# Kernel optimization log

Measured on AMD Instinct MI355X. Metric: run time of the kernel, lower is better.

## Reference

```python
import jax, jax.numpy as jnp
import numpy as np

B, N, L, D, V = 1024, 50, 50, 128, 500000
STEPS = 1  # args['n_layers']


def setup_inputs() -> dict:
    key = jax.random.key(0)
    ks = jax.random.split(key, 26)
    s = 1.0 / np.sqrt(D)  # SRGNN._init_weights uniform(-stdv, stdv)
    u = lambda k, shape: jax.random.uniform(k, shape, jnp.float32, -s, s)
    return {
        'items': jax.random.randint(ks[0], (B, N), 0, V),
        'A': jax.random.uniform(ks[1], (B, N, 2 * N), jnp.float32),
        'alias_inputs': jax.random.randint(ks[2], (B, L), 0, N),
        'mask': jnp.ones((B, L), dtype=bool),
        'lens': jax.random.randint(ks[3], (B,), 1, L + 1),
        'emb': u(ks[4], (V, D)),
        'w_ih': u(ks[5], (3 * D, 2 * D)),
        'w_hh': u(ks[6], (3 * D, D)),
        'b_ih': u(ks[7], (3 * D,)),
        'b_hh': u(ks[8], (3 * D,)),
        'b_iah': u(ks[9], (D,)),
        'b_oah': u(ks[10], (D,)),
        'w_in': u(ks[11], (D, D)),
        'bi_in': u(ks[12], (D,)),
        'w_out': u(ks[13], (D, D)),
        'bi_out': u(ks[14], (D,)),
        'w1': u(ks[15], (D, D)),
        'b1': u(ks[16], (D,)),
        'w2': u(ks[17], (D, D)),
        'b2': u(ks[18], (D,)),
        'w3': u(ks[19], (D, D)),
        'b3': u(ks[20], (D,)),
        'wt': u(ks[21], (D, 2 * D)),
        'bt': u(ks[22], (D,)),
    }


def reference(items, A, alias_inputs, mask, lens, emb, w_ih, w_hh, b_ih, b_hh,
              b_iah, b_oah, w_in, bi_in, w_out, bi_out, w1, b1, w2, b2, w3, b3,
              wt, bt):
    hidden = emb[items]  # [B, N, D]
    a_in, a_out = A[:, :, :N], A[:, :, N:]
    for _ in range(STEPS):
        # gated GNN cell (GRU-style)
        inp_in = jnp.einsum('bij,bjd->bid', a_in, hidden @ w_in.T + bi_in) + b_iah
        inp_out = jnp.einsum('bij,bjd->bid', a_out, hidden @ w_out.T + bi_out) + b_oah
        gi = jnp.concatenate([inp_in, inp_out], axis=-1) @ w_ih.T + b_ih  # [B,N,3D]
        gh = hidden @ w_hh.T + b_hh  # [B,N,3D]
        i_r, i_i, i_n = jnp.split(gi, 3, axis=-1)
        h_r, h_i, h_n = jnp.split(gh, 3, axis=-1)
        resetgate = jax.nn.sigmoid(i_r + h_r)
        inputgate = jax.nn.sigmoid(i_i + h_i)
        newgate = jnp.tanh(i_n + resetgate * h_n)
        hidden = newgate + inputgate * (hidden - newgate)
    # gather per-position node hidden states
    seq_hidden = jnp.take_along_axis(hidden, alias_inputs[:, :, None], axis=1)  # [B,L,D]
    # last valid item
    ht = jnp.take_along_axis(seq_hidden, (lens - 1)[:, None, None], axis=1)[:, 0, :]  # [B,D]
    # sigmoid attention combine
    q1 = (ht @ w1.T + b1)[:, None, :]            # [B,1,D]
    q2 = seq_hidden @ w2.T + b2                  # [B,L,D]
    alp = jax.nn.sigmoid(q1 + q2) @ w3.T + b3    # [B,L,D]
    a = jnp.sum(alp * seq_hidden * mask[:, :, None].astype(jnp.float32), axis=1)
    seq_output = jnp.concatenate([a, ht], axis=-1) @ wt.T + bt  # [B,D]
    return (seq_hidden, seq_output)
```

## Files before the change

### kernel.cpp

```cpp
#include <hip/hip_runtime.h>
#include <math.h>

#define TB 512

typedef __attribute__((ext_vector_type(8))) short bf16x8;
typedef __attribute__((ext_vector_type(4))) float f32x4;

__device__ __forceinline__ float u2f(unsigned short u){
  union { unsigned int i; float f; } v; v.i = ((unsigned int)u) << 16; return v.f;
}
__device__ __forceinline__ unsigned short f2u(float f){
  union { float ff; unsigned int i; } v; v.ff = f;
  unsigned int x = v.i;
  x += 0x7fff + ((x >> 16) & 1);
  return (unsigned short)(x >> 16);
}
__device__ __forceinline__ float sigm(float x){
  return __builtin_amdgcn_rcpf(1.0f + __expf(-x));
}
__device__ __forceinline__ float ftanh(float x){
  return 1.0f - 2.0f*__builtin_amdgcn_rcpf(1.0f + __expf(2.0f*x));
}

#define SH 136
#define ST 72
#define OFF_H    0
#define OFF_II   6800
#define OFF_IO   13600
#define OFF_HT   20400
#define OFF_AIN  29616
#define OFF_AOUT 33216
#define POOL_SZ  37824

#define WOFF_IN   0
#define WOFF_OUT  16384
#define WOFF_IH   32768
#define WOFF_HH   131072
#define WOFF_W2   180224
#define WOFF_W3   196608
#define WTOT      212992

__device__ __forceinline__ f32x4 mfma16(bf16x8 a, bf16x8 b, f32x4 c){
  return __builtin_amdgcn_mfma_f32_16x16x32_bf16(a, b, c, 0, 0, 0);
}

__device__ __forceinline__ bf16x8 cvt8(const float* __restrict__ p){
  const float4 a = *(const float4*)p;
  const float4 c = *(const float4*)(p + 4);
  bf16x8 r;
  r[0]=(short)f2u(a.x); r[1]=(short)f2u(a.y); r[2]=(short)f2u(a.z); r[3]=(short)f2u(a.w);
  r[4]=(short)f2u(c.x); r[5]=(short)f2u(c.y); r[6]=(short)f2u(c.z); r[7]=(short)f2u(c.w);
  return r;
}

__device__ __forceinline__ void gemm_frag(const unsigned short* sA, int lda,
                                          const unsigned short* sB, int ldb,
                                          int n0, int lane, int nk, f32x4 acc[4]){
  const int l15 = lane & 15, q = lane >> 4;
  for (int ks = 0; ks < nk; ++ks){
    const int k0 = ks*32 + q*8;
    bf16x8 bfr = *(const bf16x8*)(sB + (n0 + l15)*ldb + k0);
    #pragma unroll
    for (int mt = 0; mt < 4; ++mt){
      bf16x8 afr = *(const bf16x8*)(sA + (mt*16 + l15)*lda + k0);
      acc[mt] = mfma16(afr, bfr, acc[mt]);
    }
  }
}

__device__ __forceinline__ void gemm_fragB(const unsigned short* sA, int lda,
                                           const unsigned short* __restrict__ Wb, int ldw,
                                           int n0, int lane, int nk, f32x4 acc[4]){
  const int l15 = lane & 15, q = lane >> 4;
  const unsigned short* wr = Wb + (n0 + l15)*ldw;
  for (int ks = 0; ks < nk; ++ks){
    const int k0 = ks*32 + q*8;
    bf16x8 bfr = *(const bf16x8*)(wr + k0);
    #pragma unroll
    for (int mt = 0; mt < 4; ++mt){
      bf16x8 afr = *(const bf16x8*)(sA + (mt*16 + l15)*lda + k0);
      acc[mt] = mfma16(afr, bfr, acc[mt]);
    }
  }
}

__device__ __forceinline__ void gemm_fragG(const unsigned short* sA, int lda,
                                           const float* __restrict__ W, int ldw,
                                           int n0, int lane, int nk, f32x4 acc[4]){
  const int l15 = lane & 15, q = lane >> 4;
  const float* wr = W + (n0 + l15)*ldw;
  for (int ks = 0; ks < nk; ++ks){
    const int k0 = ks*32 + q*8;
    bf16x8 bfr = cvt8(wr + k0);
    #pragma unroll
    for (int mt = 0; mt < 4; ++mt){
      bf16x8 afr = *(const bf16x8*)(sA + (mt*16 + l15)*lda + k0);
      acc[mt] = mfma16(afr, bfr, acc[mt]);
    }
  }
}

__global__ void prep_weights(const float* __restrict__ w_in, const float* __restrict__ w_out,
                             const float* __restrict__ w_ih, const float* __restrict__ w_hh,
                             const float* __restrict__ w2,   const float* __restrict__ w3,
                             unsigned short* __restrict__ ws){
  const int i = blockIdx.x*blockDim.x + threadIdx.x;
  const int s = gridDim.x*blockDim.x;
  for (int e = i; e < 16384; e += s) ws[WOFF_IN  + e] = f2u(w_in[e]);
  for (int e = i; e < 16384; e += s) ws[WOFF_OUT + e] = f2u(w_out[e]);
  for (int e = i; e < 98304; e += s) ws[WOFF_IH  + e] = f2u(w_ih[e]);
  for (int e = i; e < 49152; e += s) ws[WOFF_HH  + e] = f2u(w_hh[e]);
  for (int e = i; e < 16384; e += s) ws[WOFF_W2  + e] = f2u(w2[e]);
  for (int e = i; e < 16384; e += s) ws[WOFF_W3  + e] = f2u(w3[e]);
}

template<bool WS>
__global__ __launch_bounds__(TB, 4) void srgnn_kernel(
    const int* __restrict__ items, const float* __restrict__ A,
    const int* __restrict__ alias_in, const int* __restrict__ lens,
    const float* __restrict__ emb,
    const float* __restrict__ w_ih, const float* __restrict__ w_hh,
    const float* __restrict__ b_ih, const float* __restrict__ b_hh,
    const float* __restrict__ b_iah, const float* __restrict__ b_oah,
    const float* __restrict__ w_in, const float* __restrict__ bi_in,
    const float* __restrict__ w_out, const float* __restrict__ bi_out,
    const float* __restrict__ w1, const float* __restrict__ b1,
    const float* __restrict__ w2, const float* __restrict__ b2,
    const float* __restrict__ w3, const float* __restrict__ b3,
    const float* __restrict__ wt, const float* __restrict__ bt,
    const unsigned short* __restrict__ wbf,
    float* __restrict__ out0, float* __restrict__ out1)
{
  __shared__ __align__(16) unsigned short pool[POOL_SZ];

  const int b    = blockIdx.x;
  const int tid  = threadIdx.x;
  const int lane = tid & 63;
  const int w    = tid >> 6;
  const int n0   = w << 4;
  const int l15  = lane & 15, q = lane >> 4;
  const int d    = n0 + l15;

  unsigned short* pH   = pool + OFF_H;
  unsigned short* pII  = pool + OFF_II;
  unsigned short* pIO  = pool + OFF_IO;
  unsigned short* pHT  = pool + OFF_HT;
  unsigned short* pAin = pool + OFF_AIN;
  unsigned short* pAout= pool + OFF_AOUT;
  unsigned short* pHn  = pool + OFF_AIN;
  float* sQ1  = (float*)(pool + OFF_HT);
  float* sAvec = sQ1 + 128;
  float* sAred = sQ1 + 256;

  for (int e = tid; e < 1792; e += TB){
    int r_ = e/14; pHT[r_*ST + 50 + (e - r_*14)] = 0;
  }
  for (int e = tid; e < 700; e += TB){
    int r_ = e/14, c = 50 + (e - r_*14);
    pAin[r_*ST + c] = 0; pAout[r_*ST + c] = 0;
  }

  for (int e = tid; e < 1250; e += TB){
    int i = e/25, j4 = (e - i*25) << 2;
    const float4 v = *(const float4*)(A + (long long)b*5000 + i*100 + j4);
    const float vv[4] = {v.x, v.y, v.z, v.w};
    #pragma unroll
    for (int t = 0; t < 4; ++t){
      int j = j4 + t;
      if (j < 50) pAin[i*ST + j] = f2u(vv[t]);
      else        pAout[i*ST + j - 50] = f2u(vv[t]);
    }
  }
  for (int e = tid; e < 1600; e += TB){
    int n = e >> 5, c4 = (e & 31) << 2;
    const float4 v = *(const float4*)(emb + (long long)items[b*50 + n]*128 + c4);
    unsigned short* p = pH + n*SH + c4;
    p[0] = f2u(v.x); p[1] = f2u(v.y); p[2] = f2u(v.z); p[3] = f2u(v.w);
  }
  __syncthreads();

  f32x4 acc[4];

  { const float bi = bi_in[d];
    #pragma unroll
    for (int mt = 0; mt < 4; ++mt) acc[mt] = (f32x4){bi,bi,bi,bi};
    if (WS) gemm_fragB(pH, SH, wbf + WOFF_IN, 128, n0, lane, 4, acc);
    else    gemm_fragG(pH, SH, w_in, 128, n0, lane, 4, acc);
    #pragma unroll
    for (int mt = 0; mt < 4; ++mt)
      #pragma unroll
      for (int r = 0; r < 4; ++r){
        int tok = mt*16 + q*4 + r;
        if (tok < 50) pHT[d*ST + tok] = f2u(acc[mt][r]);
      }
  }
  { const float bi = b_iah[d];
    #pragma unroll
    for (int mt = 0; mt < 4; ++mt) acc[mt] = (f32x4){bi,bi,bi,bi};
    gemm_frag(pAin, ST, pHT, ST, n0, lane, 2, acc);
    #pragma unroll
    for (int mt = 0; mt < 4; ++mt)
      #pragma unroll
      for (int r = 0; r < 4; ++r){
        int tok = mt*16 + q*4 + r;
        if (tok < 50) pII[tok*SH + d] = f2u(acc[mt][r]);
      }
  }
  { const float bi = bi_out[d];
    #pragma unroll
    for (int mt = 0; mt < 4; ++mt) acc[mt] = (f32x4){bi,bi,bi,bi};
    if (WS) gemm_fragB(pH, SH, wbf + WOFF_OUT, 128, n0, lane, 4, acc);
    else    gemm_fragG(pH, SH, w_out, 128, n0, lane, 4, acc);
    #pragma unroll
    for (int mt = 0; mt < 4; ++mt)
      #pragma unroll
      for (int r = 0; r < 4; ++r){
        int tok = mt*16 + q*4 + r;
        if (tok < 50) pHT[d*ST + tok] = f2u(acc[mt][r]);
      }
  }
  { const float bi = b_oah[d];
    #pragma unroll
    for (int mt = 0; mt < 4; ++mt) acc[mt] = (f32x4){bi,bi,bi,bi};
    gemm_frag(pAout, ST, pHT, ST, n0, lane, 2, acc);
    #pragma unroll
    for (int mt = 0; mt < 4; ++mt)
      #pragma unroll
      for (int r = 0; r < 4; ++r){
        int tok = mt*16 + q*4 + r;
        if (tok < 50) pIO[tok*SH + d] = f2u(acc[mt][r]);
      }
  }
  __syncthreads();

  unsigned int Rp[8], Zp[8];
  for (int g = 0; g < 3; ++g){
    f32x4 agi[4], agh[4];
    { const float bii = b_ih[g*128 + d], bhh = b_hh[g*128 + d];
      #pragma unroll
      for (int mt = 0; mt < 4; ++mt){
        agi[mt] = (f32x4){bii,bii,bii,bii};
        agh[mt] = (f32x4){bhh,bhh,bhh,bhh};
      }
    }
    if (WS){
      gemm_fragB(pII, SH, wbf + WOFF_IH + g*128*256,       256, n0, lane, 4, agi);
      gemm_fragB(pIO, SH, wbf + WOFF_IH + g*128*256 + 128, 256, n0, lane, 4, agi);
      gemm_fragB(pH,  SH, wbf + WOFF_HH + g*128*128,       128, n0, lane, 4, agh);
    } else {
      gemm_fragG(pII, SH, w_ih + g*128*256,       256, n0, lane, 4, agi);
      gemm_fragG(pIO, SH, w_ih + g*128*256 + 128, 256, n0, lane, 4, agi);
      gemm_fragG(pH,  SH, w_hh + g*128*128,       128, n0, lane, 4, agh);
    }

    #pragma unroll
    for (int mt = 0; mt < 4; ++mt)
      #pragma unroll
      for (int r2 = 0; r2 < 2; ++r2){
        const int p = mt*2 + r2;
        if (g == 0){
          float v0 = sigm(agi[mt][2*r2]   + agh[mt][2*r2]);
          float v1 = sigm(agi[mt][2*r2+1] + agh[mt][2*r2+1]);
          Rp[p] = (unsigned)f2u(v0) | ((unsigned)f2u(v1) << 16);
        } else if (g == 1){
          float v0 = sigm(agi[mt][2*r2]   + agh[mt][2*r2]);
          float v1 = sigm(agi[mt][2*r2+1] + agh[mt][2*r2+1]);
          Zp[p] = (unsigned)f2u(v0) | ((unsigned)f2u(v1) << 16);
        } else {
          #pragma unroll
          for (int rr = 0; rr < 2; ++rr){
            const int r = 2*r2 + rr;
            const int tok = mt*16 + q*4 + r;
            if (tok < 50){
              float Rv = u2f((unsigned short)(Rp[p] >> (rr*16)));
              float Zv = u2f((unsigned short)(Zp[p] >> (rr*16)));
              float h  = u2f(pH[tok*SH + d]);
              float ng = ftanh(agi[mt][r] + Rv*agh[mt][r]);
              pHn[tok*128 + d] = f2u(ng + Zv*(h - ng));
            }
          }
        }
      }
  }
  __syncthreads();

  for (int e = tid; e < 1600; e += TB){
    int l = e >> 5, c4 = (e & 31) << 2;
    const uint2 v = *(const uint2*)(pHn + alias_in[b*50 + l]*128 + c4);
    *(uint2*)(pH + l*SH + c4) = v;
    float4 o;
    o.x = u2f((unsigned short)(v.x)); o.y = u2f((unsigned short)(v.x >> 16));
    o.z = u2f((unsigned short)(v.y)); o.w = u2f((unsigned short)(v.y >> 16));
    *(float4*)(out0 + (long long)b*6400 + 4*e) = o;
  }
  const int hl = lens[b] - 1;
  __syncthreads();

  if (tid < 128){
    float q1v = b1[tid];
    for (int k = 0; k < 128; k += 4){
      const float4 wv = *(const float4*)(w1 + tid*128 + k);
      q1v += wv.x*u2f(pH[hl*SH + k])   + wv.y*u2f(pH[hl*SH + k+1])
           + wv.z*u2f(pH[hl*SH + k+2]) + wv.w*u2f(pH[hl*SH + k+3]);
    }
    sQ1[tid] = q1v;
  }
  { const float bi = b2[d];
    #pragma unroll
    for (int mt = 0; mt < 4; ++mt) acc[mt] = (f32x4){bi,bi,bi,bi};
    if (WS) gemm_fragB(pH, SH, wbf + WOFF_W2, 128, n0, lane, 4, acc);
    else    gemm_fragG(pH, SH, w2, 128, n0, lane, 4, acc);
    __syncthreads();
    const float q1v = sQ1[d];
    #pragma unroll
    for (int mt = 0; mt < 4; ++mt)
      #pragma unroll
      for (int r = 0; r < 4; ++r){
        int tok = mt*16 + q*4 + r;
        if (tok < 50) pII[tok*SH + d] = f2u(sigm(q1v + acc[mt][r]));
      }
  }
  __syncthreads();

  { const float bi = b3[d];
    #pragma unroll
    for (int mt = 0; mt < 4; ++mt) acc[mt] = (f32x4){bi,bi,bi,bi};
    if (WS) gemm_fragB(pII, SH, wbf + WOFF_W3, 128, n0, lane, 4, acc);
    else    gemm_fragG(pII, SH, w3, 128, n0, lane, 4, acc);
    float pa = 0.f;
    #pragma unroll
    for (int mt = 0; mt < 4; ++mt)
      #pragma unroll
      for (int r = 0; r < 4; ++r){
        int tok = mt*16 + q*4 + r;
        if (tok < 50) pa += acc[mt][r] * u2f(pH[tok*SH + d]);
      }
    pa += __shfl_xor(pa, 16);
    pa += __shfl_xor(pa, 32);
    if (lane < 16) sAvec[n0 + lane] = pa;
  }
  __syncthreads();

  { const int dd = tid & 127, gg = tid >> 7;
    float part = (gg == 0) ? bt[dd] : 0.f;
    if (gg < 2){
      for (int kk = 0; kk < 64; kk += 4){
        int k = gg*64 + kk;
        const float4 wv = *(const float4*)(wt + dd*256 + k);
        part += wv.x*sAvec[k] + wv.y*sAvec[k+1] + wv.z*sAvec[k+2] + wv.w*sAvec[k+3];
      }
    } else {
      for (int kk = 0; kk < 64; kk += 4){
        int k = (gg - 2)*64 + kk;
        const float4 wv = *(const float4*)(wt + dd*256 + 128 + k);
        part += wv.x*u2f(pH[hl*SH + k])   + wv.y*u2f(pH[hl*SH + k+1])
              + wv.z*u2f(pH[hl*SH + k+2]) + wv.w*u2f(pH[hl*SH + k+3]);
      }
    }
    sAred[gg*128 + dd] = part;
  }
  __syncthreads();
  if (tid < 128)
    out1[(long long)b*128 + tid] = sAred[tid] + sAred[128+tid] + sAred[256+tid] + sAred[384+tid];
}

extern "C" void kernel_launch(void* const* d_in, const int* in_sizes, int n_in,
                              void* d_out, int out_size, void* d_ws, size_t ws_size,
                              hipStream_t stream){
  float* out0 = (float*)d_out;
  float* out1 = out0 + 1024LL*50*128;
  const bool ws_ok = (d_ws != nullptr) && (ws_size >= (size_t)WTOT*2);
  if (ws_ok){
    prep_weights<<<256, 256, 0, stream>>>(
        (const float*)d_in[12], (const float*)d_in[14],
        (const float*)d_in[6],  (const float*)d_in[7],
        (const float*)d_in[18], (const float*)d_in[20],
        (unsigned short*)d_ws);
    srgnn_kernel<true><<<1024, TB, 0, stream>>>(
        (const int*)d_in[0], (const float*)d_in[1], (const int*)d_in[2],
        (const int*)d_in[4],
        (const float*)d_in[5],
        (const float*)d_in[6], (const float*)d_in[7], (const float*)d_in[8],
        (const float*)d_in[9], (const float*)d_in[10], (const float*)d_in[11],
        (const float*)d_in[12], (const float*)d_in[13], (const float*)d_in[14],
        (const float*)d_in[15], (const float*)d_in[16], (const float*)d_in[17],
        (const float*)d_in[18], (const float*)d_in[19], (const float*)d_in[20],
        (const float*)d_in[21], (const float*)d_in[22], (const float*)d_in[23],
        (const unsigned short*)d_ws, out0, out1);
  } else {
    srgnn_kernel<false><<<1024, TB, 0, stream>>>(
        (const int*)d_in[0], (const float*)d_in[1], (const int*)d_in[2],
        (const int*)d_in[4],
        (const float*)d_in[5],
        (const float*)d_in[6], (const float*)d_in[7], (const float*)d_in[8],
        (const float*)d_in[9], (const float*)d_in[10], (const float*)d_in[11],
        (const float*)d_in[12], (const float*)d_in[13], (const float*)d_in[14],
        (const float*)d_in[15], (const float*)d_in[16], (const float*)d_in[17],
        (const float*)d_in[18], (const float*)d_in[19], (const float*)d_in[20],
        (const float*)d_in[21], (const float*)d_in[22], (const float*)d_in[23],
        nullptr, out0, out1);
  }
}
```

Baseline: 465.8 us.

## Double block size and split token tiles across two wave groups

```diff
diff --git a/kernel.cpp b/kernel.cpp
--- a/kernel.cpp
+++ b/kernel.cpp
@@ -1,7 +1,7 @@
 #include <hip/hip_runtime.h>
 #include <math.h>
 
-#define TB 512
+#define TB 1024
 
 typedef __attribute__((ext_vector_type(8))) short bf16x8;
 typedef __attribute__((ext_vector_type(4))) float f32x4;
@@ -53,49 +53,47 @@
   return r;
 }
 
-__device__ __forceinline__ void gemm_frag(const unsigned short* sA, int lda,
-                                          const unsigned short* sB, int ldb,
-                                          int n0, int lane, int nk, f32x4 acc[4]){
+__device__ __forceinline__ void gemm2L(const unsigned short* sA, int lda, int mbase,
+                                       const unsigned short* sB, int ldb,
+                                       int n0, int lane, int nk, f32x4 acc[2]){
   const int l15 = lane & 15, q = lane >> 4;
   for (int ks = 0; ks < nk; ++ks){
     const int k0 = ks*32 + q*8;
     bf16x8 bfr = *(const bf16x8*)(sB + (n0 + l15)*ldb + k0);
     #pragma unroll
-    for (int mt = 0; mt < 4; ++mt){
-      bf16x8 afr = *(const bf16x8*)(sA + (mt*16 + l15)*lda + k0);
-      acc[mt] = mfma16(afr, bfr, acc[mt]);
-    }
-  }
-}
-
-__device__ __forceinline__ void gemm_fragB(const unsigned short* sA, int lda,
-                                           const unsigned short* __restrict__ Wb, int ldw,
-                                           int n0, int lane, int nk, f32x4 acc[4]){
+    for (int mtl = 0; mtl < 2; ++mtl){
+      bf16x8 afr = *(const bf16x8*)(sA + (mbase + mtl*16 + l15)*lda + k0);
+      acc[mtl] = mfma16(afr, bfr, acc[mtl]);
+    }
+  }
+}
+__device__ __forceinline__ void gemm2B(const unsigned short* sA, int lda, int mbase,
+                                       const unsigned short* __restrict__ Wb, int ldw,
+                                       int n0, int lane, int nk, f32x4 acc[2]){
   const int l15 = lane & 15, q = lane >> 4;
   const unsigned short* wr = Wb + (n0 + l15)*ldw;
   for (int ks = 0; ks < nk; ++ks){
     const int k0 = ks*32 + q*8;
     bf16x8 bfr = *(const bf16x8*)(wr + k0);
     #pragma unroll
-    for (int mt = 0; mt < 4; ++mt){
-      bf16x8 afr = *(const bf16x8*)(sA + (mt*16 + l15)*lda + k0);
-      acc[mt] = mfma16(afr, bfr, acc[mt]);
-    }
-  }
-}
-
-__device__ __forceinline__ void gemm_fragG(const unsigned short* sA, int lda,
-                                           const float* __restrict__ W, int ldw,
-                                           int n0, int lane, int nk, f32x4 acc[4]){
+    for (int mtl = 0; mtl < 2; ++mtl){
+      bf16x8 afr = *(const bf16x8*)(sA + (mbase + mtl*16 + l15)*lda + k0);
+      acc[mtl] = mfma16(afr, bfr, acc[mtl]);
+    }
+  }
+}
+__device__ __forceinline__ void gemm2G(const unsigned short* sA, int lda, int mbase,
+                                       const float* __restrict__ W, int ldw,
+                                       int n0, int lane, int nk, f32x4 acc[2]){
   const int l15 = lane & 15, q = lane >> 4;
   const float* wr = W + (n0 + l15)*ldw;
   for (int ks = 0; ks < nk; ++ks){
     const int k0 = ks*32 + q*8;
     bf16x8 bfr = cvt8(wr + k0);
     #pragma unroll
-    for (int mt = 0; mt < 4; ++mt){
-      bf16x8 afr = *(const bf16x8*)(sA + (mt*16 + l15)*lda + k0);
-      acc[mt] = mfma16(afr, bfr, acc[mt]);
+    for (int mtl = 0; mtl < 2; ++mtl){
+      bf16x8 afr = *(const bf16x8*)(sA + (mbase + mtl*16 + l15)*lda + k0);
+      acc[mtl] = mfma16(afr, bfr, acc[mtl]);
     }
   }
 }
@@ -115,7 +113,7 @@
 }
 
 template<bool WS>
-__global__ __launch_bounds__(TB, 4) void srgnn_kernel(
+__global__ __launch_bounds__(TB, 8) void srgnn_kernel(
     const int* __restrict__ items, const float* __restrict__ A,
     const int* __restrict__ alias_in, const int* __restrict__ lens,
     const float* __restrict__ emb,
@@ -137,7 +135,9 @@
   const int tid  = threadIdx.x;
   const int lane = tid & 63;
   const int w    = tid >> 6;
-  const int n0   = w << 4;
+  const int n0   = (w & 7) << 4;
+  const int mh   = w >> 3;
+  const int mbase= mh << 5;
   const int l15  = lane & 15, q = lane >> 4;
   const int d    = n0 + l15;
 
@@ -148,9 +148,10 @@
   unsigned short* pAin = pool + OFF_AIN;
   unsigned short* pAout= pool + OFF_AOUT;
   unsigned short* pHn  = pool + OFF_AIN;
-  float* sQ1  = (float*)(pool + OFF_HT);
-  float* sAvec = sQ1 + 128;
-  float* sAred = sQ1 + 256;
+  float* sQ1   = (float*)(pool + OFF_HT);
+  float* sAvec0= sQ1 + 128;
+  float* sAvec1= sQ1 + 256;
+  float* sAred = sQ1 + 384;
 
   for (int e = tid; e < 1792; e += TB){
     int r_ = e/14; pHT[r_*ST + 50 + (e - r_*14)] = 0;
@@ -179,103 +180,130 @@
   }
   __syncthreads();
 
-  f32x4 acc[4];
-
-  { const float bi = bi_in[d];
-    #pragma unroll
-    for (int mt = 0; mt < 4; ++mt) acc[mt] = (f32x4){bi,bi,bi,bi};
-    if (WS) gemm_fragB(pH, SH, wbf + WOFF_IN, 128, n0, lane, 4, acc);
-    else    gemm_fragG(pH, SH, w_in, 128, n0, lane, 4, acc);
-    #pragma unroll
-    for (int mt = 0; mt < 4; ++mt)
-      #pragma unroll
-      for (int r = 0; r < 4; ++r){
-        int tok = mt*16 + q*4 + r;
-        if (tok < 50) pHT[d*ST + tok] = f2u(acc[mt][r]);
-      }
-  }
+  f32x4 acc[2];
+
+  f32x4 aO[2];
+  { const float biI = bi_in[d], biO = bi_out[d];
+    acc[0] = (f32x4){biI,biI,biI,biI}; acc[1] = acc[0];
+    aO[0]  = (f32x4){biO,biO,biO,biO}; aO[1]  = aO[0];
+    if (WS){
+      const unsigned short* wI = wbf + WOFF_IN  + (n0 + l15)*128;
+      const unsigned short* wO = wbf + WOFF_OUT + (n0 + l15)*128;
+      #pragma unroll
+      for (int ks = 0; ks < 4; ++ks){
+        const int k0 = ks*32 + q*8;
+        bf16x8 bI = *(const bf16x8*)(wI + k0);
+        bf16x8 bO = *(const bf16x8*)(wO + k0);
+        #pragma unroll
+        for (int mtl = 0; mtl < 2; ++mtl){
+          bf16x8 afr = *(const bf16x8*)(pH + (mbase + mtl*16 + l15)*SH + k0);
+          acc[mtl] = mfma16(afr, bI, acc[mtl]);
+          aO[mtl]  = mfma16(afr, bO, aO[mtl]);
+        }
+      }
+    } else {
+      const float* wI = w_in  + (n0 + l15)*128;
+      const float* wO = w_out + (n0 + l15)*128;
+      #pragma unroll
+      for (int ks = 0; ks < 4; ++ks){
+        const int k0 = ks*32 + q*8;
+        bf16x8 bI = cvt8(wI + k0);
+        bf16x8 bO = cvt8(wO + k0);
+        #pragma unroll
+        for (int mtl = 0; mtl < 2; ++mtl){
+          bf16x8 afr = *(const bf16x8*)(pH + (mbase + mtl*16 + l15)*SH + k0);
+          acc[mtl] = mfma16(afr, bI, acc[mtl]);
+          aO[mtl]  = mfma16(afr, bO, aO[mtl]);
+        }
+      }
+    }
+    #pragma unroll
+    for (int mtl = 0; mtl < 2; ++mtl)
+      #pragma unroll
+      for (int r = 0; r < 4; ++r){
+        int tok = mbase + mtl*16 + q*4 + r;
+        if (tok < 50) pHT[d*ST + tok] = f2u(acc[mtl][r]);
+      }
+  }
+  __syncthreads();
+
   { const float bi = b_iah[d];
-    #pragma unroll
-    for (int mt = 0; mt < 4; ++mt) acc[mt] = (f32x4){bi,bi,bi,bi};
-    gemm_frag(pAin, ST, pHT, ST, n0, lane, 2, acc);
-    #pragma unroll
-    for (int mt = 0; mt < 4; ++mt)
-      #pragma unroll
-      for (int r = 0; r < 4; ++r){
-        int tok = mt*16 + q*4 + r;
-        if (tok < 50) pII[tok*SH + d] = f2u(acc[mt][r]);
-      }
-  }
-  { const float bi = bi_out[d];
-    #pragma unroll
-    for (int mt = 0; mt < 4; ++mt) acc[mt] = (f32x4){bi,bi,bi,bi};
-    if (WS) gemm_fragB(pH, SH, wbf + WOFF_OUT, 128, n0, lane, 4, acc);
-    else    gemm_fragG(pH, SH, w_out, 128, n0, lane, 4, acc);
-    #pragma unroll
-    for (int mt = 0; mt < 4; ++mt)
-      #pragma unroll
-      for (int r = 0; r < 4; ++r){
-        int tok = mt*16 + q*4 + r;
-        if (tok < 50) pHT[d*ST + tok] = f2u(acc[mt][r]);
-      }
-  }
+    acc[0] = (f32x4){bi,bi,bi,bi}; acc[1] = acc[0];
+    gemm2L(pAin, ST, mbase, pHT, ST, n0, lane, 2, acc);
+    #pragma unroll
+    for (int mtl = 0; mtl < 2; ++mtl)
+      #pragma unroll
+      for (int r = 0; r < 4; ++r){
+        int tok = mbase + mtl*16 + q*4 + r;
+        if (tok < 50) pII[tok*SH + d] = f2u(acc[mtl][r]);
+      }
+  }
+  __syncthreads();
+
+  {
+    #pragma unroll
+    for (int mtl = 0; mtl < 2; ++mtl)
+      #pragma unroll
+      for (int r = 0; r < 4; ++r){
+        int tok = mbase + mtl*16 + q*4 + r;
+        if (tok < 50) pHT[d*ST + tok] = f2u(aO[mtl][r]);
+      }
+  }
+  __syncthreads();
+
   { const float bi = b_oah[d];
-    #pragma unroll
-    for (int mt = 0; mt < 4; ++mt) acc[mt] = (f32x4){bi,bi,bi,bi};
-    gemm_frag(pAout, ST, pHT, ST, n0, lane, 2, acc);
-    #pragma unroll
-    for (int mt = 0; mt < 4; ++mt)
-      #pragma unroll
-      for (int r = 0; r < 4; ++r){
-        int tok = mt*16 + q*4 + r;
-        if (tok < 50) pIO[tok*SH + d] = f2u(acc[mt][r]);
-      }
-  }
-  __syncthreads();
-
-  unsigned int Rp[8], Zp[8];
+    acc[0] = (f32x4){bi,bi,bi,bi}; acc[1] = acc[0];
+    gemm2L(pAout, ST, mbase, pHT, ST, n0, lane, 2, acc);
+    #pragma unroll
+    for (int mtl = 0; mtl < 2; ++mtl)
+      #pragma unroll
+      for (int r = 0; r < 4; ++r){
+        int tok = mbase + mtl*16 + q*4 + r;
+        if (tok < 50) pIO[tok*SH + d] = f2u(acc[mtl][r]);
+      }
+  }
+  __syncthreads();
+
+  unsigned int Rp[4], Zp[4];
   for (int g = 0; g < 3; ++g){
-    f32x4 agi[4], agh[4];
+    f32x4 agi[2], agh[2];
     { const float bii = b_ih[g*128 + d], bhh = b_hh[g*128 + d];
-      #pragma unroll
-      for (int mt = 0; mt < 4; ++mt){
-        agi[mt] = (f32x4){bii,bii,bii,bii};
-        agh[mt] = (f32x4){bhh,bhh,bhh,bhh};
-      }
+      agi[0] = (f32x4){bii,bii,bii,bii}; agi[1] = agi[0];
+      agh[0] = (f32x4){bhh,bhh,bhh,bhh}; agh[1] = agh[0];
     }
     if (WS){
-      gemm_fragB(pII, SH, wbf + WOFF_IH + g*128*256,       256, n0, lane, 4, agi);
-      gemm_fragB(pIO, SH, wbf + WOFF_IH + g*128*256 + 128, 256, n0, lane, 4, agi);
-      gemm_fragB(pH,  SH, wbf + WOFF_HH + g*128*128,       128, n0, lane, 4, agh);
+      gemm2B(pII, SH, mbase, wbf + WOFF_IH + g*128*256,       256, n0, lane, 4, agi);
+      gemm2B(pIO, SH, mbase, wbf + WOFF_IH + g*128*256 + 128, 256, n0, lane, 4, agi);
+      gemm2B(pH,  SH, mbase, wbf + WOFF_HH + g*128*128,       128, n0, lane, 4, agh);
     } else {
-      gemm_fragG(pII, SH, w_ih + g*128*256,       256, n0, lane, 4, agi);
-      gemm_fragG(pIO, SH, w_ih + g*128*256 + 128, 256, n0, lane, 4, agi);
-      gemm_fragG(pH,  SH, w_hh + g*128*128,       128, n0, lane, 4, agh);
-    }
-
-    #pragma unroll
-    for (int mt = 0; mt < 4; ++mt)
+      gemm2G(pII, SH, mbase, w_ih + g*128*256,       256, n0, lane, 4, agi);
+      gemm2G(pIO, SH, mbase, w_ih + g*128*256 + 128, 256, n0, lane, 4, agi);
+      gemm2G(pH,  SH, mbase, w_hh + g*128*128,       128, n0, lane, 4, agh);
+    }
+
+    #pragma unroll
+    for (int mtl = 0; mtl < 2; ++mtl)
       #pragma unroll
       for (int r2 = 0; r2 < 2; ++r2){
-        const int p = mt*2 + r2;
+        const int p = mtl*2 + r2;
         if (g == 0){
-          float v0 = sigm(agi[mt][2*r2]   + agh[mt][2*r2]);
-          float v1 = sigm(agi[mt][2*r2+1] + agh[mt][2*r2+1]);
+          float v0 = sigm(agi[mtl][2*r2]   + agh[mtl][2*r2]);
+          float v1 = sigm(agi[mtl][2*r2+1] + agh[mtl][2*r2+1]);
           Rp[p] = (unsigned)f2u(v0) | ((unsigned)f2u(v1) << 16);
         } else if (g == 1){
-          float v0 = sigm(agi[mt][2*r2]   + agh[mt][2*r2]);
-          float v1 = sigm(agi[mt][2*r2+1] + agh[mt][2*r2+1]);
+          float v0 = sigm(agi[mtl][2*r2]   + agh[mtl][2*r2]);
+          float v1 = sigm(agi[mtl][2*r2+1] + agh[mtl][2*r2+1]);
           Zp[p] = (unsigned)f2u(v0) | ((unsigned)f2u(v1) << 16);
         } else {
           #pragma unroll
           for (int rr = 0; rr < 2; ++rr){
             const int r = 2*r2 + rr;
-            const int tok = mt*16 + q*4 + r;
+            const int tok = mbase + mtl*16 + q*4 + r;
             if (tok < 50){
               float Rv = u2f((unsigned short)(Rp[p] >> (rr*16)));
               float Zv = u2f((unsigned short)(Zp[p] >> (rr*16)));
               float h  = u2f(pH[tok*SH + d]);
-              float ng = ftanh(agi[mt][r] + Rv*agh[mt][r]);
+              float ng = ftanh(agi[mtl][r] + Rv*agh[mtl][r]);
               pHn[tok*128 + d] = f2u(ng + Zv*(h - ng));
             }
           }
@@ -306,52 +334,54 @@
     sQ1[tid] = q1v;
   }
   { const float bi = b2[d];
-    #pragma unroll
-    for (int mt = 0; mt < 4; ++mt) acc[mt] = (f32x4){bi,bi,bi,bi};
-    if (WS) gemm_fragB(pH, SH, wbf + WOFF_W2, 128, n0, lane, 4, acc);
-    else    gemm_fragG(pH, SH, w2, 128, n0, lane, 4, acc);
+    acc[0] = (f32x4){bi,bi,bi,bi}; acc[1] = acc[0];
+    if (WS) gemm2B(pH, SH, mbase, wbf + WOFF_W2, 128, n0, lane, 4, acc);
+    else    gemm2G(pH, SH, mbase, w2, 128, n0, lane, 4, acc);
     __syncthreads();
     const float q1v = sQ1[d];
     #pragma unroll
-    for (int mt = 0; mt < 4; ++mt)
-      #pragma unroll
-      for (int r = 0; r < 4; ++r){
-        int tok = mt*16 + q*4 + r;
-        if (tok < 50) pII[tok*SH + d] = f2u(sigm(q1v + acc[mt][r]));
+    for (int mtl = 0; mtl < 2; ++mtl)
+      #pragma unroll
+      for (int r = 0; r < 4; ++r){
+        int tok = mbase + mtl*16 + q*4 + r;
+        if (tok < 50) pII[tok*SH + d] = f2u(sigm(q1v + acc[mtl][r]));
       }
   }
   __syncthreads();
 
   { const float bi = b3[d];
-    #pragma unroll
-    for (int mt = 0; mt < 4; ++mt) acc[mt] = (f32x4){bi,bi,bi,bi};
-    if (WS) gemm_fragB(pII, SH, wbf + WOFF_W3, 128, n0, lane, 4, acc);
-    else    gemm_fragG(pII, SH, w3, 128, n0, lane, 4, acc);
+    acc[0] = (f32x4){bi,bi,bi,bi}; acc[1] = acc[0];
+    if (WS) gemm2B(pII, SH, mbase, wbf + WOFF_W3, 128, n0, lane, 4, acc);
+    else    gemm2G(pII, SH, mbase, w3, 128, n0, lane, 4, acc);
     float pa = 0.f;
     #pragma unroll
-    for (int mt = 0; mt < 4; ++mt)
-      #pragma unroll
-      for (int r = 0; r < 4; ++r){
-        int tok = mt*16 + q*4 + r;
-        if (tok < 50) pa += acc[mt][r] * u2f(pH[tok*SH + d]);
+    for (int mtl = 0; mtl < 2; ++mtl)
+      #pragma unroll
+      for (int r = 0; r < 4; ++r){
+        int tok = mbase + mtl*16 + q*4 + r;
+        if (tok < 50) pa += acc[mtl][r] * u2f(pH[tok*SH + d]);
       }
     pa += __shfl_xor(pa, 16);
     pa += __shfl_xor(pa, 32);
-    if (lane < 16) sAvec[n0 + lane] = pa;
+    if (lane < 16){
+      if (mh == 0) sAvec0[n0 + lane] = pa;
+      else         sAvec1[n0 + lane] = pa;
+    }
   }
   __syncthreads();
 
   { const int dd = tid & 127, gg = tid >> 7;
     float part = (gg == 0) ? bt[dd] : 0.f;
-    if (gg < 2){
-      for (int kk = 0; kk < 64; kk += 4){
-        int k = gg*64 + kk;
+    if (gg < 4){
+      for (int kk = 0; kk < 32; kk += 4){
+        int k = gg*32 + kk;
         const float4 wv = *(const float4*)(wt + dd*256 + k);
-        part += wv.x*sAvec[k] + wv.y*sAvec[k+1] + wv.z*sAvec[k+2] + wv.w*sAvec[k+3];
+        part += wv.x*(sAvec0[k]  +sAvec1[k])   + wv.y*(sAvec0[k+1]+sAvec1[k+1])
+              + wv.z*(sAvec0[k+2]+sAvec1[k+2]) + wv.w*(sAvec0[k+3]+sAvec1[k+3]);
       }
     } else {
-      for (int kk = 0; kk < 64; kk += 4){
-        int k = (gg - 2)*64 + kk;
+      for (int kk = 0; kk < 32; kk += 4){
+        int k = (gg - 4)*32 + kk;
         const float4 wv = *(const float4*)(wt + dd*256 + 128 + k);
         part += wv.x*u2f(pH[hl*SH + k])   + wv.y*u2f(pH[hl*SH + k+1])
               + wv.z*u2f(pH[hl*SH + k+2]) + wv.w*u2f(pH[hl*SH + k+3]);
@@ -360,8 +390,12 @@
     sAred[gg*128 + dd] = part;
   }
   __syncthreads();
-  if (tid < 128)
-    out1[(long long)b*128 + tid] = sAred[tid] + sAred[128+tid] + sAred[256+tid] + sAred[384+tid];
+  if (tid < 128){
+    float s = 0.f;
+    #pragma unroll
+    for (int gg = 0; gg < 8; ++gg) s += sAred[gg*128 + tid];
+    out1[(long long)b*128 + tid] = s;
+  }
 }
 
 extern "C" void kernel_launch(void* const* d_in, const int* in_sizes, int n_in,
```

After: 509.3 us. 9.4% more time.
